# Kernel optimization log

Hardware: AMD Instinct MI355X
Metric: run time of the kernel (lower is better)

The kernel has to match this reference:

```python
import jax, jax.numpy as jnp
import numpy as np

DEGREE = 3
N_BASIS = 16


def _clamped_knots(n_basis, degree):
    # Clamped uniform knot vector on [0, 1]: degree+1 repeated knots at each end.
    n_interior = n_basis - degree - 1
    interior = np.linspace(0.0, 1.0, n_interior + 2)[1:-1]
    knots = np.concatenate([np.zeros(degree + 1), interior, np.ones(degree + 1)])
    return jnp.asarray(knots, dtype=jnp.float32)


def bspline_basis(x, degree=DEGREE, n_basis=N_BASIS):
    # Cox-de Boor recursion, vectorized over all leading dims of x.
    # x: (...,) in [0,1] -> (..., n_basis)
    t = _clamped_knots(n_basis, degree)
    n_knots = n_basis + degree + 1
    xe = jnp.clip(x, 0.0, 1.0 - 1e-6)[..., None]
    B = ((xe >= t[:-1]) & (xe < t[1:])).astype(x.dtype)  # (..., n_knots-1)
    for p in range(1, degree + 1):
        dl = t[p:n_knots - 1] - t[:n_knots - 1 - p]
        dr = t[p + 1:n_knots] - t[1:n_knots - p]
        left = jnp.where(dl > 0, (xe - t[:n_knots - 1 - p]) / jnp.where(dl > 0, dl, 1.0), 0.0)
        right = jnp.where(dr > 0, (t[p + 1:n_knots] - xe) / jnp.where(dr > 0, dr, 1.0), 0.0)
        B = left * B[..., :-1] + right * B[..., 1:]
    return B  # (..., n_basis)


def _kl(cm, lv):
    # KL(N(cm, exp(lv)) || N(0, 1)) summed over all edges/coeffs (prior_scale = 1).
    var = jnp.exp(lv)
    return 0.5 * jnp.sum(var + cm * cm - 1.0 - lv)


def _layer(x, cm, lv):
    # x: (B, in); cm, lv: (out, in, n_basis)
    basis = bspline_basis(x)  # (B, in, n_basis)
    out = jnp.einsum('bik,oik->bo', basis, cm)  # fused per-edge weighted sum
    return out, _kl(cm, lv)


def setup_inputs() -> dict:
    key = jax.random.key(0)
    ks = jax.random.split(key, 4)
    B = 8192
    sizes = [256, 512, 512, 256]
    nb = N_BASIS
    inp = {"x": jax.random.uniform(ks[0], (B, sizes[0]), dtype=jnp.float32)}
    for i in range(3):
        inp[f"cm{i}"] = 0.1 * jax.random.normal(ks[1 + i], (sizes[i + 1], sizes[i], nb), dtype=jnp.float32)
        inp[f"lv{i}"] = -2.0 * jnp.ones((sizes[i + 1], sizes[i], nb), dtype=jnp.float32)
    return inp


def reference(x, cm0, lv0, cm1, lv1, cm2, lv2):
    out = x
    kl = jnp.zeros((), x.dtype)
    for cm, lv in ((cm0, lv0), (cm1, lv1), (cm2, lv2)):
        out, k = _layer(out, cm, lv)
        kl = kl + k
    return out, kl
```

## Files before the change

### kernel.cpp

```cpp
#include <hip/hip_runtime.h>
#include <hip/hip_bf16.h>


typedef __attribute__((ext_vector_type(8))) _Float16 f16x8;
typedef __attribute__((ext_vector_type(4))) float float4v;
typedef unsigned short ushort_t;

#define GLOBAL_AS __attribute__((address_space(1)))
#define LDS_AS __attribute__((address_space(3)))

__device__ __forceinline__ void async_copy16(const void* g, void* l) {
  __builtin_amdgcn_global_load_lds((const GLOBAL_AS unsigned int*)g,
                                   (LDS_AS unsigned int*)l, 16, 0, 0);
}

__device__ __forceinline__ ushort_t f2h(float f) {
  _Float16 h = (_Float16)f;
  return *(ushort_t*)&h;
}
__device__ __forceinline__ float h2f(ushort_t u) {
  return (float)*(_Float16*)&u;
}

__device__ __forceinline__ void bspline_w4(float x, int& k0, float w[4]) {
  const float XMAX = 1.0f - 1e-6f;
  float xe = fminf(fmaxf(x, 0.0f), XMAX);
  int cell = (int)(xe * 13.0f);
  cell = cell > 12 ? 12 : cell;
  k0 = cell;
  int j = cell + 3;
  const float s = 1.0f / 13.0f;
  int cjm2 = max(j - 5, 0);
  int cjm1 = max(j - 4, 0);
  int cj   = j - 3;
  int cj1  = j - 2;
  int cj2  = min(j - 1, 13);
  int cj3  = min(j, 13);
  float tjm2 = cjm2 * s, tjm1 = cjm1 * s, tj = cj * s;
  float tj1 = cj1 * s, tj2 = cj2 * s, tj3 = cj3 * s;
  float left1 = xe - tj, left2 = xe - tjm1, left3 = xe - tjm2;
  float right1 = tj1 - xe, right2 = tj2 - xe, right3 = tj3 - xe;
#define INV3(d) ((d) == 1 ? 13.0f : ((d) == 2 ? 6.5f : (13.0f / 3.0f)))
  float i10 = INV3(cj1 - cj);
  float i20 = INV3(cj1 - cjm1), i21 = INV3(cj2 - cj);
  float i30 = INV3(cj1 - cjm2), i31 = INV3(cj2 - cjm1), i32 = INV3(cj3 - cj);
#undef INV3
  float temp = i10;
  float N0 = right1 * temp;
  float N1 = left1 * temp;
  temp = N0 * i20;
  N0 = right1 * temp;
  float saved = left2 * temp;
  temp = N1 * i21;
  N1 = saved + right2 * temp;
  float N2 = left1 * temp;
  temp = N0 * i30;
  N0 = right1 * temp;
  saved = left3 * temp;
  temp = N1 * i31;
  N1 = saved + right2 * temp;
  saved = left2 * temp;
  temp = N2 * i32;
  N2 = saved + right3 * temp;
  float N3 = left1 * temp;
  w[0] = N0; w[1] = N1; w[2] = N2; w[3] = N3;
}

__device__ __forceinline__ void compose16(const float w[4], int k0, unsigned u[8]) {
  unsigned h0 = f2h(w[0]), h1 = f2h(w[1]), h2 = f2h(w[2]), h3 = f2h(w[3]);
  int e = k0 >> 1;
  bool odd = (k0 & 1) != 0;
  unsigned a = odd ? (h0 << 16) : (h0 | (h1 << 16));
  unsigned b = odd ? (h1 | (h2 << 16)) : (h2 | (h3 << 16));
  unsigned c = odd ? (unsigned)h3 : 0u;
#pragma unroll
  for (int j = 0; j < 8; ++j)
    u[j] = (j == e) ? a : (j == e + 1) ? b : (j == e + 2) ? c : 0u;
}

template <bool SPLIT_A>
__global__ __launch_bounds__(256, 2) void kan_layer(
    const float* __restrict__ act, const ushort_t* __restrict__ Bsw,
    float* __restrict__ outp, int IN, int OUT) {
  const int K = IN * 16;
  const int KC = K >> 3;
  __shared__ ushort_t Bt[32 * 512];
  __shared__ ushort_t Ahi[16 * 512];
  __shared__ ushort_t Alo[SPLIT_A ? 16 * 512 : 1];

  const int tid = threadIdx.x;
  const int lane = tid & 63;
  const int wv = tid >> 6;
  const int wm = wv >> 1, wn = wv & 1;
  const int quad = lane >> 4, l15 = lane & 15;
  const int b0 = blockIdx.x * 128;
  const int n0 = blockIdx.y * 256;
  const int tbase = n0 >> 4;

  float4v acc[4][8];
#pragma unroll
  for (int a = 0; a < 4; a++)
#pragma unroll
    for (int b = 0; b < 8; b++) acc[a][b] = (float4v)0.0f;

  const int sr = tid & 127;
  const int sf = (tid >> 7) * 2;

  const int nsteps = K / 64;
  const int chunk = nsteps / gridDim.z;
  const int kbeg = blockIdx.z * chunk;
  const int kend = kbeg + chunk;

  for (int kstep = kbeg; kstep < kend; ++kstep) {
    const float2 xv = *(const float2*)&act[(size_t)(b0 + sr) * IN + kstep * 4 + sf];
    unsigned uh0[8], uh1[8], ul0[8], ul1[8];
    {
      int k0; float w[4];
      bspline_w4(xv.x, k0, w);
      compose16(w, k0, uh0);
      if (SPLIT_A) {
        float wl[4];
#pragma unroll
        for (int t = 0; t < 4; ++t) wl[t] = w[t] - h2f(f2h(w[t]));
        compose16(wl, k0, ul0);
      }
      bspline_w4(xv.y, k0, w);
      compose16(w, k0, uh1);
      if (SPLIT_A) {
        float wl[4];
#pragma unroll
        for (int t = 0; t < 4; ++t) wl[t] = w[t] - h2f(f2h(w[t]));
        compose16(wl, k0, ul1);
      }
    }

    __syncthreads();

#pragma unroll
    for (int j = 0; j < 8; ++j) {
      int w = wv * 8 + j;
      int nt = w >> 1, kc = w & 1;
      size_t goff = ((size_t)(tbase + nt) * KC + (size_t)kstep * 8 + kc * 4) * 128
                    + lane * 8;
      async_copy16(&Bsw[goff], &Bt[w * 512 + lane * 8]);
    }

#pragma unroll
    for (int f = 0; f < 2; ++f) {
      const unsigned* uh = f == 0 ? uh0 : uh1;
      int ff = sf + f;
      int base = ((sr >> 4) * 2 + (ff >> 1)) * 512 + (ff & 1) * 256 + (sr & 15) * 8;
      *(uint4*)&Ahi[base]       = make_uint4(uh[0], uh[1], uh[2], uh[3]);
      *(uint4*)&Ahi[base + 128] = make_uint4(uh[4], uh[5], uh[6], uh[7]);
      if (SPLIT_A) {
        const unsigned* ul = f == 0 ? ul0 : ul1;
        *(uint4*)&Alo[base]       = make_uint4(ul[0], ul[1], ul[2], ul[3]);
        *(uint4*)&Alo[base + 128] = make_uint4(ul[4], ul[5], ul[6], ul[7]);
      }
    }

    __syncthreads();

#pragma unroll
    for (int ks = 0; ks < 2; ++ks) {
      f16x8 ah[4], al[4], bh[8];
#pragma unroll
      for (int mt = 0; mt < 4; ++mt) {
        int fb = ((wm * 4 + mt) * 2 + ks) * 512 + lane * 8;
        ah[mt] = *(const f16x8*)&Ahi[fb];
        if (SPLIT_A) al[mt] = *(const f16x8*)&Alo[fb];
      }
#pragma unroll
      for (int nt = 0; nt < 8; ++nt)
        bh[nt] = *(const f16x8*)&Bt[((wn * 8 + nt) * 2 + ks) * 512 + lane * 8];
#pragma unroll
      for (int mt = 0; mt < 4; ++mt)
#pragma unroll
        for (int nt = 0; nt < 8; ++nt) {
          if (SPLIT_A)
            acc[mt][nt] = __builtin_amdgcn_mfma_f32_16x16x32_f16(al[mt], bh[nt], acc[mt][nt], 0, 0, 0);
          acc[mt][nt] = __builtin_amdgcn_mfma_f32_16x16x32_f16(ah[mt], bh[nt], acc[mt][nt], 0, 0, 0);
        }
    }
  }

#pragma unroll
  for (int mt = 0; mt < 4; ++mt)
#pragma unroll
    for (int nt = 0; nt < 8; ++nt) {
      int col = n0 + wn * 128 + nt * 16 + l15;
#pragma unroll
      for (int r = 0; r < 4; ++r) {
        int row = b0 + wm * 64 + mt * 16 + quad * 4 + r;
        atomicAdd(&outp[(size_t)row * OUT + col], acc[mt][nt][r]);
      }
    }
}

__global__ __launch_bounds__(256) void kl_convert(
    const float* __restrict__ cm, const float* __restrict__ lv,
    ushort_t* __restrict__ bsw, int G ,
    long long ngroups, float* __restrict__ klout) {
  long long i = (long long)blockIdx.x * blockDim.x + threadIdx.x;
  const long long stride = (long long)gridDim.x * blockDim.x;
  float s = 0.0f;
  for (; i < ngroups; i += stride) {
    int o = (int)(i / G);
    int kc = (int)(i - (long long)o * G);
    const float* cp = &cm[i * 8];
    const float* lp = &lv[i * 8];
    unsigned pk[4];
#pragma unroll
    for (int t = 0; t < 4; ++t) {
      float c0 = cp[2 * t], c1 = cp[2 * t + 1];
      float l0 = lp[2 * t], l1 = lp[2 * t + 1];
      pk[t] = (unsigned)f2h(c0) | ((unsigned)f2h(c1) << 16);
      s += 0.5f * (__expf(l0) + c0 * c0 - 1.0f - l0);
      s += 0.5f * (__expf(l1) + c1 * c1 - 1.0f - l1);
    }
    uint4 v; v.x = pk[0]; v.y = pk[1]; v.z = pk[2]; v.w = pk[3];
    size_t doff = (((size_t)(o >> 4) * G + kc) * 16 + (o & 15)) * 8;
    *(uint4*)&bsw[doff] = v;
  }
#pragma unroll
  for (int off = 32; off > 0; off >>= 1) s += __shfl_down(s, off, 64);
  __shared__ float red[4];
  int wvi = threadIdx.x >> 6;
  if ((threadIdx.x & 63) == 0) red[wvi] = s;
  __syncthreads();
  if (threadIdx.x == 0)
    atomicAdd(klout, red[0] + red[1] + red[2] + red[3]);
}

extern "C" void kernel_launch(void* const* d_in, const int* in_sizes, int n_in,
                              void* d_out, int out_size, void* d_ws, size_t ws_size,
                              hipStream_t stream) {
  const float* x   = (const float*)d_in[0];
  const float* cm0 = (const float*)d_in[1];
  const float* lv0 = (const float*)d_in[2];
  const float* cm1 = (const float*)d_in[3];
  const float* lv1 = (const float*)d_in[4];
  const float* cm2 = (const float*)d_in[5];
  const float* lv2 = (const float*)d_in[6];

  float* out = (float*)d_out;
  float* klp = out + (size_t)8192 * 256;

  char* ws = (char*)d_ws;
  float*    act1 = (float*)(ws);
  float*    act2 = (float*)(ws + ((size_t)16 << 20));
  ushort_t* b0sw = (ushort_t*)(ws + ((size_t)32 << 20));
  ushort_t* b1sw = (ushort_t*)(ws + ((size_t)36 << 20));
  ushort_t* b2sw = (ushort_t*)(ws + ((size_t)44 << 20));

  hipMemsetAsync(ws, 0, (size_t)32 << 20, stream);
  hipMemsetAsync(d_out, 0, (size_t)out_size * sizeof(float), stream);

  kl_convert<<<2048, 256, 0, stream>>>(cm0, lv0, b0sw, 256 * 2, 512LL * 256 * 2, klp);
  kl_convert<<<2048, 256, 0, stream>>>(cm1, lv1, b1sw, 512 * 2, 512LL * 512 * 2, klp);
  kl_convert<<<2048, 256, 0, stream>>>(cm2, lv2, b2sw, 512 * 2, 256LL * 512 * 2, klp);

  kan_layer<true ><<<dim3(64, 2, 4), 256, 0, stream>>>(x,    b0sw, act1, 256, 512);
  kan_layer<false><<<dim3(64, 2, 4), 256, 0, stream>>>(act1, b1sw, act2, 512, 512);
  kan_layer<false><<<dim3(64, 1, 8), 256, 0, stream>>>(act2, b2sw, out,  512, 256);
}
```

Before: 515.5 us.

## Double-buffer B tiles and prefetch next activation in KAN layer GEMM

```diff
diff --git a/kernel.cpp b/kernel.cpp
--- a/kernel.cpp
+++ b/kernel.cpp
@@ -84,9 +84,9 @@
     float* __restrict__ outp, int IN, int OUT) {
   const int K = IN * 16;
   const int KC = K >> 3;
-  __shared__ ushort_t Bt[32 * 512];
-  __shared__ ushort_t Ahi[16 * 512];
-  __shared__ ushort_t Alo[SPLIT_A ? 16 * 512 : 1];
+  __shared__ ushort_t Bt[2][16 * 512];
+  __shared__ ushort_t Ahi[8 * 512];
+  __shared__ ushort_t Alo[SPLIT_A ? 8 * 512 : 1];
 
   const int tid = threadIdx.x;
   const int lane = tid & 63;
@@ -104,75 +104,73 @@
     for (int b = 0; b < 8; b++) acc[a][b] = (float4v)0.0f;
 
   const int sr = tid & 127;
-  const int sf = (tid >> 7) * 2;
-
-  const int nsteps = K / 64;
+  const int sf = tid >> 7;
+  const int awoff = (sr >> 4) * 512 + sf * 256 + (sr & 15) * 8;
+
+  const int nsteps = K / 32;
   const int chunk = nsteps / gridDim.z;
   const int kbeg = blockIdx.z * chunk;
   const int kend = kbeg + chunk;
 
-  for (int kstep = kbeg; kstep < kend; ++kstep) {
-    const float2 xv = *(const float2*)&act[(size_t)(b0 + sr) * IN + kstep * 4 + sf];
-    unsigned uh0[8], uh1[8], ul0[8], ul1[8];
+#define ISSUE_B(kk, buf)                                                      \
+  {                                                                           \
+    _Pragma("unroll") for (int j = 0; j < 4; ++j) {                           \
+      int w = wv * 4 + j;                                                     \
+      size_t goff =                                                           \
+          ((size_t)(tbase + w) * KC + (size_t)(kk) * 4) * 128 + lane * 8;     \
+      async_copy16(&Bsw[goff], &Bt[buf][w * 512 + lane * 8]);                 \
+    }                                                                         \
+  }
+
+  int k0c; float wc[4];
+  {
+    float x0 = act[(size_t)(b0 + sr) * IN + kbeg * 2 + sf];
+    bspline_w4(x0, k0c, wc);
+  }
+  ISSUE_B(kbeg, 0);
+  float xnext = (kbeg + 1 < kend)
+                    ? act[(size_t)(b0 + sr) * IN + (kbeg + 1) * 2 + sf]
+                    : 0.0f;
+
+  for (int k = kbeg; k < kend; ++k) {
+    const int buf = (k - kbeg) & 1;
+
+    __syncthreads();
+
     {
-      int k0; float w[4];
-      bspline_w4(xv.x, k0, w);
-      compose16(w, k0, uh0);
+      unsigned u[8];
+      compose16(wc, k0c, u);
+      *(uint4*)&Ahi[awoff]       = make_uint4(u[0], u[1], u[2], u[3]);
+      *(uint4*)&Ahi[awoff + 128] = make_uint4(u[4], u[5], u[6], u[7]);
       if (SPLIT_A) {
         float wl[4];
 #pragma unroll
-        for (int t = 0; t < 4; ++t) wl[t] = w[t] - h2f(f2h(w[t]));
-        compose16(wl, k0, ul0);
+        for (int t = 0; t < 4; ++t) wl[t] = wc[t] - h2f(f2h(wc[t]));
+        compose16(wl, k0c, u);
+        *(uint4*)&Alo[awoff]       = make_uint4(u[0], u[1], u[2], u[3]);
+        *(uint4*)&Alo[awoff + 128] = make_uint4(u[4], u[5], u[6], u[7]);
       }
-      bspline_w4(xv.y, k0, w);
-      compose16(w, k0, uh1);
-      if (SPLIT_A) {
-        float wl[4];
-#pragma unroll
-        for (int t = 0; t < 4; ++t) wl[t] = w[t] - h2f(f2h(w[t]));
-        compose16(wl, k0, ul1);
-      }
-    }
+    }
+
+    bspline_w4(xnext, k0c, wc);
 
     __syncthreads();
 
-#pragma unroll
-    for (int j = 0; j < 8; ++j) {
-      int w = wv * 8 + j;
-      int nt = w >> 1, kc = w & 1;
-      size_t goff = ((size_t)(tbase + nt) * KC + (size_t)kstep * 8 + kc * 4) * 128
-                    + lane * 8;
-      async_copy16(&Bsw[goff], &Bt[w * 512 + lane * 8]);
-    }
-
-#pragma unroll
-    for (int f = 0; f < 2; ++f) {
-      const unsigned* uh = f == 0 ? uh0 : uh1;
-      int ff = sf + f;
-      int base = ((sr >> 4) * 2 + (ff >> 1)) * 512 + (ff & 1) * 256 + (sr & 15) * 8;
-      *(uint4*)&Ahi[base]       = make_uint4(uh[0], uh[1], uh[2], uh[3]);
-      *(uint4*)&Ahi[base + 128] = make_uint4(uh[4], uh[5], uh[6], uh[7]);
-      if (SPLIT_A) {
-        const unsigned* ul = f == 0 ? ul0 : ul1;
-        *(uint4*)&Alo[base]       = make_uint4(ul[0], ul[1], ul[2], ul[3]);
-        *(uint4*)&Alo[base + 128] = make_uint4(ul[4], ul[5], ul[6], ul[7]);
-      }
-    }
-
-    __syncthreads();
-
-#pragma unroll
-    for (int ks = 0; ks < 2; ++ks) {
+    if (k + 1 < kend) ISSUE_B(k + 1, buf ^ 1);
+    if (k + 2 < kend)
+      xnext = act[(size_t)(b0 + sr) * IN + (k + 2) * 2 + sf];
+
+    {
       f16x8 ah[4], al[4], bh[8];
 #pragma unroll
       for (int mt = 0; mt < 4; ++mt) {
-        int fb = ((wm * 4 + mt) * 2 + ks) * 512 + lane * 8;
+        int fb = (wm * 4 + mt) * 512 + lane * 8;
         ah[mt] = *(const f16x8*)&Ahi[fb];
         if (SPLIT_A) al[mt] = *(const f16x8*)&Alo[fb];
       }
 #pragma unroll
       for (int nt = 0; nt < 8; ++nt)
-        bh[nt] = *(const f16x8*)&Bt[((wn * 8 + nt) * 2 + ks) * 512 + lane * 8];
+        bh[nt] = *(const f16x8*)&Bt[buf][(wn * 8 + nt) * 512 + lane * 8];
 #pragma unroll
       for (int mt = 0; mt < 4; ++mt)
 #pragma unroll
@@ -183,6 +181,7 @@
         }
     }
   }
+#undef ISSUE_B
 
 #pragma unroll
   for (int mt = 0; mt < 4; ++mt)
```

Measured after the change: 535.7 us. 1.04x slower.
